# Kernel tuning notes

Measured on AMD Instinct MI355X. Metric: run time of the kernel, lower is better.

Reference implementation:

```python
import jax, jax.numpy as jnp
import numpy as np

B, S, H, A, M, V, E = 128, 64, 1000, 1000, 500, 30000, 620


def setup_inputs() -> dict:
    key = jax.random.key(0)
    ks = jax.random.split(key, 20)
    sc = 0.02
    return {
        "x": jax.random.randint(ks[0], (B, 1), 0, V),
        "hidden": jax.random.normal(ks[1], (B, H), jnp.float32),
        "outputs": jax.random.normal(ks[2], (B, S, 2 * H), jnp.float32),
        "emb": jax.random.normal(ks[3], (V, E), jnp.float32) * sc,
        "W_hp": jax.random.normal(ks[4], (A, H), jnp.float32) * sc,
        "b_hp": jnp.zeros((A,), jnp.float32),
        "W_op": jax.random.normal(ks[5], (A, 2 * H), jnp.float32) * sc,
        "b_op": jnp.zeros((A,), jnp.float32),
        "v_e": jax.random.normal(ks[6], (A,), jnp.float32) * sc,
        "W_ih": jax.random.normal(ks[7], (3 * H, 2 * H + E), jnp.float32) * sc,
        "W_hh": jax.random.normal(ks[8], (3 * H, H), jnp.float32) * sc,
        "b_ih": jnp.zeros((3 * H,), jnp.float32),
        "b_hh": jnp.zeros((3 * H,), jnp.float32),
        "W_wv": jax.random.normal(ks[9], (2 * M, 2 * H), jnp.float32) * sc,
        "b_wv": jnp.zeros((2 * M,), jnp.float32),
        "W_lh": jax.random.normal(ks[10], (2 * M, H), jnp.float32) * sc,
        "b_lh": jnp.zeros((2 * M,), jnp.float32),
        "W_le": jax.random.normal(ks[11], (2 * M, E), jnp.float32) * sc,
        "b_le": jnp.zeros((2 * M,), jnp.float32),
        "W_pred": jax.random.normal(ks[12], (V, M), jnp.float32) * sc,
        "b_pred": jnp.zeros((V,), jnp.float32),
    }


def reference(x, hidden, outputs, emb, W_hp, b_hp, W_op, b_op, v_e,
              W_ih, W_hh, b_ih, b_hh, W_wv, b_wv, W_lh, b_lh, W_le, b_le,
              W_pred, b_pred):
    # --- Bahdanau attention (broadcast instead of repeat) ---
    h_proj = hidden @ W_hp.T + b_hp                      # [B,A]
    o_proj = jnp.einsum('bsk,ak->bsa', outputs, W_op) + b_op  # [B,S,A]
    energy = jnp.tanh(h_proj[:, None, :] + o_proj) @ v_e # [B,S]
    attn = jax.nn.softmax(energy, axis=1)                # [B,S]
    ctx = jnp.einsum('bs,bsk->bk', attn, outputs)        # [B,2H] weighted_values

    # --- embedding lookup ---
    emb_x = emb[x[:, 0]]                                 # [B,E]

    # --- single-step GRU (PyTorch gate layout: r, z, n) ---
    gru_in = jnp.concatenate([emb_x, ctx], axis=1)       # [B, E+2H]
    gi = gru_in @ W_ih.T + b_ih                          # [B,3H]
    gh = hidden @ W_hh.T + b_hh                          # [B,3H]
    ir, iz, inn = gi[:, :H], gi[:, H:2*H], gi[:, 2*H:]
    hr, hz, hn = gh[:, :H], gh[:, H:2*H], gh[:, 2*H:]
    r = jax.nn.sigmoid(ir + hr)
    z = jax.nn.sigmoid(iz + hz)
    n = jnp.tanh(inn + r * hn)
    h_new = (1.0 - z) * n + z * hidden                   # [B,H]

    # --- maxout combine of three linears ---
    mo_in = (hidden @ W_lh.T + b_lh) + (emb_x @ W_le.T + b_le) + (ctx @ W_wv.T + b_wv)  # [B,2M]
    mo = mo_in.reshape(-1, M, 2).max(axis=2)             # [B,M]

    prediction = mo @ W_pred.T + b_pred                  # [B,V]
    return prediction, h_new
```

## Files before the change

### kernel.cpp

```cpp
#include <hip/hip_runtime.h>
#include <hip/hip_bf16.h>
#include <math.h>

typedef short bf16x8 __attribute__((ext_vector_type(8)));
typedef float f32x4 __attribute__((ext_vector_type(4)));
typedef unsigned short us8 __attribute__((ext_vector_type(8)));
typedef unsigned short us4 __attribute__((ext_vector_type(4)));

namespace {
constexpr int B_ = 128;
constexpr int S_ = 64;
constexpr int H_ = 1000;
constexpr int A_ = 1000;
constexpr int M_ = 500;
constexpr int V_ = 30000;
constexpr int E_ = 620;

constexpr int KP_OUT  = 2048;
constexpr int KP_HP   = 1024;
constexpr int KP_PRED = 512;
constexpr int LD_CAT  = 3712;
constexpr int NP_A    = 1024;
constexpr int NP_3H   = 3072;
constexpr int OROWS   = 8192;

constexpr int Z_HP = 4, Z_GI = 6, Z_GH = 4, Z_MO = 6, Z_OP = 2;

__device__ __forceinline__ unsigned short f2b(float f) {
  __hip_bfloat16 h = __float2bfloat16(f);
  return *reinterpret_cast<unsigned short*>(&h);
}
__device__ __forceinline__ float b2f(unsigned short u) {
  unsigned v = ((unsigned)u) << 16;
  return __uint_as_float(v);
}
__device__ __forceinline__ float sigmoidf_(float x) {
  return 1.0f / (1.0f + __expf(-x));
}
__device__ __forceinline__ void load_lds16(const void* g, void* l) {
  auto gp = reinterpret_cast<const __attribute__((address_space(1))) char*>(
      reinterpret_cast<uintptr_t>(g));
  unsigned loff = (unsigned)(uintptr_t)l;
  auto lp = reinterpret_cast<__attribute__((address_space(3))) char*>(loff);
  __builtin_amdgcn_global_load_lds(gp, lp, 16, 0, 0);
}
}

struct CJob {
  const float* src; unsigned short* dst;
  int nchunks, cpr, Kel, Rs, ld, coff, Wlim, bstart, nblk;
};

__global__ __launch_bounds__(256) void megacast(CJob j0, CJob j1, CJob j2)
{
  const int bid = blockIdx.x;
  CJob j = j0;
  if (bid >= j1.bstart) j = j1;
  if (bid >= j2.bstart) j = j2;

  const int tpj = j.nblk << 8;
  const int base = ((bid - j.bstart) << 8) + (int)threadIdx.x;

  for (int i = base; i < j.nchunks; i += tpj * 2) {
    const int i2 = i + tpj;
    const bool okB = (i2 < j.nchunks);
    const int rA = i / j.cpr;
    const int cA = (i - rA * j.cpr) << 3;
    const int rB = okB ? (i2 / j.cpr) : 0;
    const int cB = okB ? ((i2 - rB * j.cpr) << 3) : 0;
    const bool fA = (rA < j.Rs) && (cA + 8 <= j.Kel);
    const bool fB = okB && (rB < j.Rs) && (cB + 8 <= j.Kel);

    float4 a0, a1, b0, b1;
    if (fA) {
      const float* s = j.src + (size_t)rA * j.Kel + cA;
      a0 = *(const float4*)s; a1 = *(const float4*)(s + 4);
    }
    if (fB) {
      const float* s = j.src + (size_t)rB * j.Kel + cB;
      b0 = *(const float4*)s; b1 = *(const float4*)(s + 4);
    }

    if (fA) {
      us8 o;
      o[0] = f2b(a0.x); o[1] = f2b(a0.y); o[2] = f2b(a0.z); o[3] = f2b(a0.w);
      o[4] = f2b(a1.x); o[5] = f2b(a1.y); o[6] = f2b(a1.z); o[7] = f2b(a1.w);
      *(us8*)(j.dst + (size_t)rA * j.ld + j.coff + cA) = o;
    } else {
      unsigned short* drow = j.dst + (size_t)rA * j.ld + j.coff;
#pragma unroll
      for (int e = 0; e < 8; ++e) {
        const int c = cA + e;
        if (c < j.Wlim) {
          const float v = (rA < j.Rs && c < j.Kel)
                              ? j.src[(size_t)rA * j.Kel + c] : 0.f;
          drow[c] = f2b(v);
        }
      }
    }
    if (okB) {
      if (fB) {
        us8 o;
        o[0] = f2b(b0.x); o[1] = f2b(b0.y); o[2] = f2b(b0.z); o[3] = f2b(b0.w);
        o[4] = f2b(b1.x); o[5] = f2b(b1.y); o[6] = f2b(b1.z); o[7] = f2b(b1.w);
        *(us8*)(j.dst + (size_t)rB * j.ld + j.coff + cB) = o;
      } else {
        unsigned short* drow = j.dst + (size_t)rB * j.ld + j.coff;
#pragma unroll
        for (int e = 0; e < 8; ++e) {
          const int c = cB + e;
          if (c < j.Wlim) {
            const float v = (rB < j.Rs && c < j.Kel)
                                ? j.src[(size_t)rB * j.Kel + c] : 0.f;
            drow[c] = f2b(v);
          }
        }
      }
    }
  }
}

struct SJob {
  const unsigned short* A; int lda;
  const float* B; int ldb;
  int Nv, Kv;
  float* C; int ldc;
  const float* bias; int Ncol;
  int nK, Z, ntiles, bstart;
};

__global__ __launch_bounds__(256, 4) void gemm_skinny(
    SJob j0, SJob j1, SJob j2, SJob j3)
{
  __shared__ __align__(16) char Bs[2][4096];

  const int bid = blockIdx.x;
  SJob j = j0;
  if (bid >= j1.bstart) j = j1;
  if (bid >= j2.bstart) j = j2;
  if (bid >= j3.bstart) j = j3;
  const int lb = bid - j.bstart;
  const int tile = lb % j.ntiles, z = lb / j.ntiles;
  const int n0 = tile * 32;
  const int ks = (int)((long)j.nK * z / j.Z);
  const int ke = (int)((long)j.nK * (z + 1) / j.Z);

  const int t = threadIdx.x, lane = t & 63, wid = t >> 6;
  const int l15 = lane & 15, l4 = lane >> 4;
  const int mrow = (wid & 1) * 64;
  const int whalf = wid >> 1;

  const int srow = t >> 3;
  const int skq = (t & 7) * 8;
  const int grow = n0 + srow;
  const bool rowok = grow < j.Nv;
  const float* Bp = j.B + (size_t)(rowok ? grow : 0) * j.ldb;
  const unsigned swcol = (unsigned)(skq * 2) ^ (((unsigned)srow & 7u) << 4);

  const unsigned short* Arow = j.A + (size_t)(mrow + l15) * j.lda + l4 * 8;
  const int brow = whalf * 16 + l15;
  const unsigned bb = (unsigned)brow * 128;
  const unsigned bsw = (((unsigned)brow & 7u) << 4);

  float4 sf0, sf1;
  auto stage_load = [&](int kst) {
    const int gk = kst * 64 + skq;
    sf0 = make_float4(0.f, 0.f, 0.f, 0.f);
    sf1 = make_float4(0.f, 0.f, 0.f, 0.f);
    if (rowok) {
      if (gk + 8 <= j.Kv) {
        sf0 = *(const float4*)(Bp + gk);
        sf1 = *(const float4*)(Bp + gk + 4);
      } else {
        float tmp[8];
#pragma unroll
        for (int e = 0; e < 8; ++e)
          tmp[e] = (gk + e < j.Kv) ? Bp[gk + e] : 0.f;
        sf0 = make_float4(tmp[0], tmp[1], tmp[2], tmp[3]);
        sf1 = make_float4(tmp[4], tmp[5], tmp[6], tmp[7]);
      }
    }
  };
  auto stage_write = [&](int buf) {
    us8 o;
    o[0] = f2b(sf0.x); o[1] = f2b(sf0.y); o[2] = f2b(sf0.z); o[3] = f2b(sf0.w);
    o[4] = f2b(sf1.x); o[5] = f2b(sf1.y); o[6] = f2b(sf1.z); o[7] = f2b(sf1.w);
    *(us8*)((char*)Bs[buf] + srow * 128 + swcol) = o;
  };

  f32x4 acc[4] = {};
  stage_load(ks);
  stage_write(0);
  __syncthreads();

  for (int kst = ks; kst < ke; ++kst) {
    const int cur = (kst - ks) & 1;
    const bool more = (kst + 1 < ke);
    if (more) stage_load(kst + 1);
    bf16x8 Af[4][2];
#pragma unroll
    for (int kk = 0; kk < 2; ++kk)
#pragma unroll
      for (int mf = 0; mf < 4; ++mf)
        Af[mf][kk] = *(const bf16x8*)(Arow + (size_t)mf * 16 * j.lda +
                                      kst * 64 + kk * 32);
    bf16x8 Bf[2];
#pragma unroll
    for (int kk = 0; kk < 2; ++kk)
      Bf[kk] = *(const bf16x8*)((char*)Bs[cur] + bb +
                                ((unsigned)(kk * 64 + l4 * 16) ^ bsw));
#pragma unroll
    for (int kk = 0; kk < 2; ++kk)
#pragma unroll
      for (int mf = 0; mf < 4; ++mf)
        acc[mf] = __builtin_amdgcn_mfma_f32_16x16x32_bf16(Af[mf][kk], Bf[kk],
                                                          acc[mf], 0, 0, 0);
    if (more) stage_write(cur ^ 1);
    __syncthreads();
  }

  const int c = n0 + whalf * 16 + l15;
  if (j.bias) {
    if (c < j.Ncol) {
      const float bv = j.bias[c];
#pragma unroll
      for (int mf = 0; mf < 4; ++mf) {
        const int r = mrow + mf * 16 + l4 * 4;
#pragma unroll
        for (int q = 0; q < 4; ++q)
          j.C[(size_t)(r + q) * j.ldc + c] = acc[mf][q] + bv;
      }
    }
  } else {
    float* Cz = j.C + (size_t)z * 128 * j.ldc;
#pragma unroll
    for (int mf = 0; mf < 4; ++mf) {
      const int r = mrow + mf * 16 + l4 * 4;
#pragma unroll
      for (int q = 0; q < 4; ++q)
        Cz[(size_t)(r + q) * j.ldc + c] = acc[mf][q];
    }
  }
}

__global__ __launch_bounds__(256, 2) void pred_gemm(
    const unsigned short* __restrict__ mo_bf,
    const float* __restrict__ Wp,
    const float* __restrict__ bias,
    float* __restrict__ C)
{
  __shared__ __align__(16) char Bs0[32768];
  __shared__ __align__(16) char Bs1[32768];

  const int t = threadIdx.x, lane = t & 63, wid = t >> 6;
  const int l15 = lane & 15, l4 = lane >> 4;
  const int n0 = blockIdx.x * 64;
  const int mrow = wid * 32;

  bf16x8 af[2][16];
#pragma unroll
  for (int ksl = 0; ksl < 16; ++ksl)
#pragma unroll
    for (int mf = 0; mf < 2; ++mf)
      af[mf][ksl] = *(const bf16x8*)(mo_bf +
          (size_t)(mrow + mf * 16 + l15) * KP_PRED + ksl * 32 + l4 * 8);

  auto stage = [&](int st, char* buf) {
#pragma unroll
    for (int i = 0; i < 8; ++i) {
      const unsigned off = (unsigned)i * 4096 + (unsigned)t * 16;
      const unsigned row = off >> 11, colb = off & 2047u;
      const unsigned sc = colb ^ ((row & 7u) << 4);
      const int rg = n0 + st * 16 + (int)row;
      const bool ok = (rg < V_) && (sc + 16 <= 2000u);
      const char* src = ok ? ((const char*)Wp + (size_t)rg * 2000 + sc)
                           : (const char*)Wp;
      load_lds16(src, buf + off);
    }
  };

  f32x4 acc[4][2] = {};

  stage(0, Bs0);
  stage(1, Bs1);

#define PWAIT(N) do {                                              \
    asm volatile("s_waitcnt vmcnt(" #N ")" ::: "memory");          \
    __builtin_amdgcn_sched_barrier(0);                             \
    __builtin_amdgcn_s_barrier();                                  \
  } while (0)

#define PCOMPUTE(T, BUF) do {                                              \
    const char* Brow_ = (const char*)(BUF) + (unsigned)l15 * 2048;         \
    const unsigned sw_ = ((unsigned)l15 & 7u) << 4;                        \
    _Pragma("unroll")                                                      \
    for (int ksl = 0; ksl < 16; ++ksl) {                                   \
      const unsigned base_ = (unsigned)(ksl * 128 + l4 * 32);              \
      const float4 f0_ = *(const float4*)(Brow_ + (base_ ^ sw_));          \
      const float4 f1_ = *(const float4*)(Brow_ + ((base_ + 16) ^ sw_));   \
      bf16x8 bf_;                                                          \
      bf_[0] = (short)f2b(f0_.x); bf_[1] = (short)f2b(f0_.y);              \
      bf_[2] = (short)f2b(f0_.z); bf_[3] = (short)f2b(f0_.w);              \
      bf_[4] = (short)f2b(f1_.x); bf_[5] = (short)f2b(f1_.y);              \
      bf_[6] = (short)f2b(f1_.z); bf_[7] = (short)f2b(f1_.w);              \
      acc[T][0] = __builtin_amdgcn_mfma_f32_16x16x32_bf16(af[0][ksl], bf_, \
                                                          acc[T][0], 0, 0, 0); \
      acc[T][1] = __builtin_amdgcn_mfma_f32_16x16x32_bf16(af[1][ksl], bf_, \
                                                          acc[T][1], 0, 0, 0); \
    }                                                                      \
  } while (0)

  PWAIT(8);
  PCOMPUTE(0, Bs0);
  __builtin_amdgcn_s_barrier();
  stage(2, Bs0);

  PWAIT(8);
  PCOMPUTE(1, Bs1);
  __builtin_amdgcn_s_barrier();
  stage(3, Bs1);

  PWAIT(8);
  PCOMPUTE(2, Bs0);

  PWAIT(0);
  PCOMPUTE(3, Bs1);

#undef PWAIT
#undef PCOMPUTE

#pragma unroll
  for (int st = 0; st < 4; ++st) {
    const int c = n0 + st * 16 + l15;
    if (c < V_) {
      const float bv = bias[c];
#pragma unroll
      for (int mf = 0; mf < 2; ++mf) {
        const int r = mrow + mf * 16 + l4 * 4;
#pragma unroll
        for (int q = 0; q < 4; ++q)
          C[(size_t)(r + q) * V_ + c] = acc[st][mf][q] + bv;
      }
    }
  }
}

__global__ __launch_bounds__(256, 4) void gemm128_part(
    const unsigned short* __restrict__ Abf, int ldA,
    const unsigned short* __restrict__ Bbf, int ldB,
    unsigned short* __restrict__ Cout, int ldc, int nK)
{
  __shared__ __align__(16) char As[16384];
  __shared__ __align__(16) char Bs[16384];

  const int t = threadIdx.x;
  const int lane = t & 63, wid = t >> 6;
  const int wm = wid >> 1, wn = wid & 1;
  const int l15 = lane & 15, l4 = lane >> 4;
  const int m0 = blockIdx.x * 128;
  const int n0 = blockIdx.y * 128;
  const int z = blockIdx.z, Z = gridDim.z;
  const int ks = (int)((long)nK * z / Z), ke = (int)((long)nK * (z + 1) / Z);

  f32x4 acc[4][4] = {};

  for (int kst = ks; kst < ke; ++kst) {
    const int k0 = kst * 64;
#pragma unroll
    for (int c = 0; c < 4; ++c) {
      const unsigned ou = c * 4096 + wid * 1024;
      const unsigned oo = ou + lane * 16;
      const unsigned row = oo >> 7, cb = oo & 127u;
      const unsigned scb = cb ^ ((row & 7u) << 4);
      load_lds16((const char*)Abf + ((size_t)(m0 + row) * ldA + k0) * 2 + scb,
                 As + ou);
    }
#pragma unroll
    for (int c = 0; c < 4; ++c) {
      const unsigned ou = c * 4096 + wid * 1024;
      const unsigned oo = ou + lane * 16;
      const unsigned row = oo >> 7, cb = oo & 127u;
      const unsigned scb = cb ^ ((row & 7u) << 4);
      load_lds16((const char*)Bbf + ((size_t)(n0 + row) * ldB + k0) * 2 + scb,
                 Bs + ou);
    }
    __syncthreads();

#pragma unroll
    for (int kk = 0; kk < 2; ++kk) {
      bf16x8 af[4], bfr[4];
#pragma unroll
      for (int i = 0; i < 4; ++i) {
        const unsigned ra = wm * 64 + i * 16 + l15;
        const unsigned ca = (unsigned)(kk * 64 + l4 * 16) ^ ((ra & 7u) << 4);
        af[i] = *(const bf16x8*)(As + ra * 128 + ca);
        const unsigned rb = wn * 64 + i * 16 + l15;
        const unsigned cb2 = (unsigned)(kk * 64 + l4 * 16) ^ ((rb & 7u) << 4);
        bfr[i] = *(const bf16x8*)(Bs + rb * 128 + cb2);
      }
#pragma unroll
      for (int i = 0; i < 4; ++i)
#pragma unroll
        for (int jj = 0; jj < 4; ++jj)
          acc[i][jj] = __builtin_amdgcn_mfma_f32_16x16x32_bf16(af[i], bfr[jj],
                                                               acc[i][jj], 0, 0, 0);
    }
    __syncthreads();
  }

  unsigned short* Cz = Cout + (size_t)z * OROWS * ldc;
#pragma unroll
  for (int i = 0; i < 4; ++i) {
    const int r = m0 + wm * 64 + i * 16 + l4 * 4;
#pragma unroll
    for (int jj = 0; jj < 4; ++jj) {
      const int c = n0 + wn * 64 + jj * 16 + l15;
#pragma unroll
      for (int q = 0; q < 4; ++q)
        Cz[(size_t)(r + q) * ldc + c] = f2b(acc[i][jj][q]);
    }
  }
}

__global__ __launch_bounds__(256) void hp_combine(
    const float* __restrict__ hp, const float* __restrict__ b_op,
    const float* __restrict__ b_hp, float* __restrict__ hpc)
{
  const int idx = blockIdx.x * 256 + threadIdx.x;
  if (idx >= B_ * NP_A) return;
  const int c = idx & (NP_A - 1);
  float s = (c < A_) ? (b_op[c] + b_hp[c]) : 0.f;
#pragma unroll
  for (int zz = 0; zz < Z_HP; ++zz) s += hp[(size_t)zz * B_ * NP_A + idx];
  hpc[idx] = s;
}

__global__ __launch_bounds__(256) void energy_reduce(
    const unsigned short* __restrict__ opart, const float* __restrict__ hpc,
    const float* __restrict__ ve, float* __restrict__ energy)
{
  const int r = blockIdx.x;
  const int b = r >> 6;
  const int t = threadIdx.x;
  float s = 0.f;
  if (t < 250) {
    const int c0 = t * 4;
    const us4 v0 = *(const us4*)(opart + (size_t)r * NP_A + c0);
    const us4 v1 = *(const us4*)(opart + (size_t)OROWS * NP_A + (size_t)r * NP_A + c0);
    const float4 h = *(const float4*)(hpc + (size_t)b * NP_A + c0);
    const float4 vv = *(const float4*)(ve + c0);
    s = tanhf(b2f(v0[0]) + b2f(v1[0]) + h.x) * vv.x
      + tanhf(b2f(v0[1]) + b2f(v1[1]) + h.y) * vv.y
      + tanhf(b2f(v0[2]) + b2f(v1[2]) + h.z) * vv.z
      + tanhf(b2f(v0[3]) + b2f(v1[3]) + h.w) * vv.w;
  }
#pragma unroll
  for (int w = 1; w < 64; w <<= 1) s += __shfl_xor(s, w);
  __shared__ float red[4];
  if ((t & 63) == 0) red[t >> 6] = s;
  __syncthreads();
  if (t == 0) energy[r] = red[0] + red[1] + red[2] + red[3];
}

__global__ __launch_bounds__(256) void softmax_ctx_cat(
    const float* __restrict__ energy, const unsigned short* __restrict__ outb,
    const float* __restrict__ hidden, const float* __restrict__ emb,
    const int* __restrict__ x, unsigned short* __restrict__ cat3)
{
  const int b = blockIdx.x, yq = blockIdx.y;
  const int t = threadIdx.x;
  __shared__ float attn[S_];
  __shared__ float sinv_s;

  if (t < 64) {
    const float e = energy[b * S_ + t];
    float m = e;
#pragma unroll
    for (int w = 1; w < 64; w <<= 1) m = fmaxf(m, __shfl_xor(m, w));
    const float p = __expf(e - m);
    float s = p;
#pragma unroll
    for (int w = 1; w < 64; w <<= 1) s += __shfl_xor(s, w);
    attn[t] = p;
    if (t == 0) sinv_s = 1.f / s;
  }
  __syncthreads();
  const float inv = sinv_s;
  unsigned short* catb = cat3 + (size_t)b * LD_CAT;

  {
    const int c0 = (250 * yq) / 4, c1 = (250 * (yq + 1)) / 4;
    const unsigned short* ob = outb + (size_t)b * S_ * KP_OUT;
    for (int kk = c0 + t; kk < c1; kk += 256) {
      float a[8] = {0.f, 0.f, 0.f, 0.f, 0.f, 0.f, 0.f, 0.f};
      for (int s = 0; s < S_; ++s) {
        const float w = attn[s];
        const us8 v = *(const us8*)(ob + (size_t)s * KP_OUT + kk * 8);
#pragma unroll
        for (int jj = 0; jj < 8; ++jj) a[jj] = fmaf(w, b2f(v[jj]), a[jj]);
      }
      us4 lo, hi;
#pragma unroll
      for (int jj = 0; jj < 4; ++jj) {
        lo[jj] = f2b(a[jj] * inv); hi[jj] = f2b(a[jj + 4] * inv);
      }
      *(us4*)(catb + 1620 + kk * 8) = lo;
      *(us4*)(catb + 1620 + kk * 8 + 4) = hi;
    }
  }
  {
    const int c0 = (250 * yq) / 4, c1 = (250 * (yq + 1)) / 4;
    for (int kk = c0 + t; kk < c1; kk += 256) {
      const float4 f = *(const float4*)(hidden + (size_t)b * H_ + kk * 4);
      us4 v; v[0] = f2b(f.x); v[1] = f2b(f.y); v[2] = f2b(f.z); v[3] = f2b(f.w);
      *(us4*)(catb + kk * 4) = v;
    }
  }
  {
    const int xi = x[b];
    const int c0 = (155 * yq) / 4, c1 = (155 * (yq + 1)) / 4;
    for (int kk = c0 + t; kk < c1; kk += 256) {
      const float4 f = *(const float4*)(emb + (size_t)xi * E_ + kk * 4);
      us4 v; v[0] = f2b(f.x); v[1] = f2b(f.y); v[2] = f2b(f.z); v[3] = f2b(f.w);
      *(us4*)(catb + 1000 + kk * 4) = v;
    }
  }
  if (yq == 3) {
    for (int kk = t; kk < 23; kk += 256) {
      us4 v; v[0] = 0; v[1] = 0; v[2] = 0; v[3] = 0;
      *(us4*)(catb + 3620 + kk * 4) = v;
    }
  }
}

__global__ __launch_bounds__(256) void gru_combine(
    const float* __restrict__ gi, const float* __restrict__ gh,
    const float* __restrict__ b_ih, const float* __restrict__ b_hh,
    const float* __restrict__ hidden, float* __restrict__ hout)
{
  const int idx = blockIdx.x * 256 + threadIdx.x;
  if (idx >= B_ * H_) return;
  const int b = idx / H_, h = idx - b * H_;
  float ir = b_ih[h], iz = b_ih[H_ + h], in = b_ih[2 * H_ + h];
  float hr = b_hh[h], hz = b_hh[H_ + h], hn = b_hh[2 * H_ + h];
#pragma unroll
  for (int zz = 0; zz < Z_GI; ++zz) {
    const float* g = gi + (size_t)zz * B_ * NP_3H + (size_t)b * NP_3H;
    ir += g[h]; iz += g[H_ + h]; in += g[2 * H_ + h];
  }
#pragma unroll
  for (int zz = 0; zz < Z_GH; ++zz) {
    const float* g = gh + (size_t)zz * B_ * NP_3H + (size_t)b * NP_3H;
    hr += g[h]; hz += g[H_ + h]; hn += g[2 * H_ + h];
  }
  const float r = sigmoidf_(ir + hr);
  const float zg = sigmoidf_(iz + hz);
  const float n = tanhf(in + r * hn);
  hout[idx] = (1.f - zg) * n + zg * hidden[idx];
}

__global__ __launch_bounds__(256) void maxpair_cast(
    const float* __restrict__ mo_in,
    const float* __restrict__ b_lh, const float* __restrict__ b_le,
    const float* __restrict__ b_wv, unsigned short* __restrict__ mo_bf)
{
  const int idx = blockIdx.x * 256 + threadIdx.x;
  if (idx >= B_ * KP_PRED) return;
  const int r = idx >> 9, c = idx & 511;
  unsigned short o = 0;
  if (c < M_) {
    const int j0 = 2 * c, j1 = 2 * c + 1;
    float v0 = b_lh[j0] + b_le[j0] + b_wv[j0];
    float v1 = b_lh[j1] + b_le[j1] + b_wv[j1];
#pragma unroll
    for (int zz = 0; zz < Z_MO; ++zz) {
      const float* g = mo_in + (size_t)zz * B_ * NP_A + (size_t)r * NP_A;
      v0 += g[j0]; v1 += g[j1];
    }
    o = f2b(fmaxf(v0, v1));
  }
  mo_bf[idx] = o;
}

extern "C" void kernel_launch(void* const* d_in, const int* in_sizes, int n_in,
                              void* d_out, int out_size, void* d_ws, size_t ws_size,
                              hipStream_t stream)
{
  const int*   x       = (const int*)  d_in[0];
  const float* hidden  = (const float*)d_in[1];
  const float* outputs = (const float*)d_in[2];
  const float* emb     = (const float*)d_in[3];
  const float* W_hp    = (const float*)d_in[4];
  const float* b_hp    = (const float*)d_in[5];
  const float* W_op    = (const float*)d_in[6];
  const float* b_op    = (const float*)d_in[7];
  const float* v_e     = (const float*)d_in[8];
  const float* W_ih    = (const float*)d_in[9];
  const float* W_hh    = (const float*)d_in[10];
  const float* b_ih    = (const float*)d_in[11];
  const float* b_hh    = (const float*)d_in[12];
  const float* W_wv    = (const float*)d_in[13];
  const float* b_wv    = (const float*)d_in[14];
  const float* W_lh    = (const float*)d_in[15];
  const float* b_lh    = (const float*)d_in[16];
  const float* W_le    = (const float*)d_in[17];
  const float* b_le    = (const float*)d_in[18];
  const float* W_pred  = (const float*)d_in[19];
  const float* b_pred  = (const float*)d_in[20];

  char* w = (char*)d_ws;
  auto alloc = [&](size_t bytes) {
    char* p = w; w += (bytes + 255) & ~(size_t)255; return p;
  };
  unsigned short* outputs_bf = (unsigned short*)alloc((size_t)OROWS * KP_OUT * 2);
  unsigned short* W_op_bf    = (unsigned short*)alloc((size_t)NP_A * KP_OUT * 2);
  unsigned short* hidden_bf  = (unsigned short*)alloc((size_t)B_ * KP_HP * 2);
  unsigned short* cat3_bf    = (unsigned short*)alloc((size_t)B_ * LD_CAT * 2);
  unsigned short* mo_bf      = (unsigned short*)alloc((size_t)B_ * KP_PRED * 2);
  float* hp     = (float*)alloc((size_t)Z_HP * B_ * NP_A * 4);
  float* hpc    = (float*)alloc((size_t)B_ * NP_A * 4);
  float* energy = (float*)alloc((size_t)B_ * S_ * 4);
  float* gh     = (float*)alloc((size_t)Z_GH * B_ * NP_3H * 4);
  char* un = w;
  unsigned short* opart = (unsigned short*)un;
  float* gi     = (float*)un;
  float* mo_in  = gi + (size_t)Z_GI * B_ * NP_3H;

  float* pred = (float*)d_out;
  float* hout = pred + (size_t)B_ * V_;

  const dim3 blk(256);
  const int FAR = 0x7fffffff;
  const SJob dummy = { nullptr, 0, nullptr, 0, 0, 0, nullptr, 0,
                       nullptr, 0, 1, 1, 1, FAR };

  {
    CJob jo  = { outputs, outputs_bf, OROWS * 256, 256, 2000, OROWS,
                 KP_OUT, 0, KP_OUT, 0,    2560 };
    CJob jwo = { W_op,    W_op_bf,    NP_A * 256,  256, 2000, A_,
                 KP_OUT, 0, KP_OUT, 2560, 320 };
    CJob jh  = { hidden,  hidden_bf,  B_ * 128,    128, 1000, B_,
                 KP_HP,  0, KP_HP,  2880, 32 };
    megacast<<<dim3(2912), blk, 0, stream>>>(jo, jwo, jh);
  }

  {
    SJob jhp = { hidden_bf, KP_HP, W_hp, H_, A_, H_, hp, NP_A,
                 nullptr, 0, 16, Z_HP, 32, 0 };
    SJob jgh = { hidden_bf, KP_HP, W_hh, H_, 3 * H_, H_, gh, NP_3H,
                 nullptr, 0, 16, Z_GH, 94, 128 };
    gemm_skinny<<<dim3(504), blk, 0, stream>>>(jhp, jgh, dummy, dummy);
  }
  hp_combine<<<dim3(B_ * NP_A / 256), blk, 0, stream>>>(hp, b_op, b_hp, hpc);

  gemm128_part<<<dim3(64, 8, Z_OP), blk, 0, stream>>>(
      outputs_bf, KP_OUT, W_op_bf, KP_OUT, opart, NP_A, KP_OUT / 64);

  energy_reduce<<<dim3(OROWS), blk, 0, stream>>>(opart, hpc, v_e, energy);

  softmax_ctx_cat<<<dim3(B_, 4), blk, 0, stream>>>(
      energy, outputs_bf, hidden, emb, x, cat3_bf);

  {
    SJob jgi = { cat3_bf + 1000, LD_CAT, W_ih, 2620, 3 * H_, 2620, gi, NP_3H,
                 nullptr, 0, 41, Z_GI, 94, 0 };
    SJob jlh = { cat3_bf, LD_CAT, W_lh, H_, A_, H_,
                 mo_in, NP_A, nullptr, 0, 16, 2, 32, 564 };
    SJob jle = { cat3_bf + 1000, LD_CAT, W_le, E_, A_, E_,
                 mo_in + (size_t)2 * B_ * NP_A, NP_A, nullptr, 0, 10, 1, 32, 628 };
    SJob jwv = { cat3_bf + 1620, LD_CAT, W_wv, 2 * H_, A_, 2 * H_,
                 mo_in + (size_t)3 * B_ * NP_A, NP_A, nullptr, 0, 32, 3, 32, 660 };
    gemm_skinny<<<dim3(756), blk, 0, stream>>>(jgi, jlh, jle, jwv);
  }

  gru_combine<<<dim3((B_ * H_ + 255) / 256), blk, 0, stream>>>(
      gi, gh, b_ih, b_hh, hidden, hout);

  maxpair_cast<<<dim3((B_ * KP_PRED + 255) / 256), blk, 0, stream>>>(
      mo_in, b_lh, b_le, b_wv, mo_bf);

  pred_gemm<<<dim3(469), blk, 0, stream>>>(mo_bf, W_pred, b_pred, pred);
}
```

Before: 161.3 us.

## Double-buffer LDS tiles in gemm128_part to overlap global loads with MFMA

Turns the split-K bf16 GEMM's single LDS buffer into two and prefetches the tile for step k+2 while step k is computed. Explicit vmcnt waits and raw s_barrier replace __syncthreads, so the load of the next tile stays in flight. LDS use per block doubles to 64KB, which lowers occupancy (launch bounds drop from 4 to 2 blocks per CU). The code always issues stage(ks+1) even when the range holds a single k-step, which could read past the intended slice.

```diff
diff --git a/kernel.cpp b/kernel.cpp
--- a/kernel.cpp
+++ b/kernel.cpp
@@ -345,13 +345,13 @@
   }
 }
 
-__global__ __launch_bounds__(256, 4) void gemm128_part(
+__global__ __launch_bounds__(256, 2) void gemm128_part(
     const unsigned short* __restrict__ Abf, int ldA,
     const unsigned short* __restrict__ Bbf, int ldB,
     unsigned short* __restrict__ Cout, int ldc, int nK)
 {
-  __shared__ __align__(16) char As[16384];
-  __shared__ __align__(16) char Bs[16384];
+  __shared__ __align__(16) char As[2][16384];
+  __shared__ __align__(16) char Bs[2][16384];
 
   const int t = threadIdx.x;
   const int lane = t & 63, wid = t >> 6;
@@ -362,9 +362,7 @@
   const int z = blockIdx.z, Z = gridDim.z;
   const int ks = (int)((long)nK * z / Z), ke = (int)((long)nK * (z + 1) / Z);
 
-  f32x4 acc[4][4] = {};
-
-  for (int kst = ks; kst < ke; ++kst) {
+  auto stage = [&](int kst, int p) {
     const int k0 = kst * 64;
 #pragma unroll
     for (int c = 0; c < 4; ++c) {
@@ -373,18 +371,26 @@
       const unsigned row = oo >> 7, cb = oo & 127u;
       const unsigned scb = cb ^ ((row & 7u) << 4);
       load_lds16((const char*)Abf + ((size_t)(m0 + row) * ldA + k0) * 2 + scb,
-                 As + ou);
-    }
-#pragma unroll
-    for (int c = 0; c < 4; ++c) {
-      const unsigned ou = c * 4096 + wid * 1024;
-      const unsigned oo = ou + lane * 16;
-      const unsigned row = oo >> 7, cb = oo & 127u;
-      const unsigned scb = cb ^ ((row & 7u) << 4);
+                 As[p] + ou);
       load_lds16((const char*)Bbf + ((size_t)(n0 + row) * ldB + k0) * 2 + scb,
-                 Bs + ou);
-    }
-    __syncthreads();
+                 Bs[p] + ou);
+    }
+  };
+
+  f32x4 acc[4][4] = {};
+
+  stage(ks, 0);
+  stage(ks + 1, 1);
+
+  for (int kst = ks; kst < ke; ++kst) {
+    const int cur = (kst - ks) & 1;
+    if (kst + 1 < ke) {
+      asm volatile("s_waitcnt vmcnt(8)" ::: "memory");
+    } else {
+      asm volatile("s_waitcnt vmcnt(0)" ::: "memory");
+    }
+    __builtin_amdgcn_sched_barrier(0);
+    __builtin_amdgcn_s_barrier();
 
 #pragma unroll
     for (int kk = 0; kk < 2; ++kk) {
@@ -393,10 +399,10 @@
       for (int i = 0; i < 4; ++i) {
         const unsigned ra = wm * 64 + i * 16 + l15;
         const unsigned ca = (unsigned)(kk * 64 + l4 * 16) ^ ((ra & 7u) << 4);
-        af[i] = *(const bf16x8*)(As + ra * 128 + ca);
+        af[i] = *(const bf16x8*)(As[cur] + ra * 128 + ca);
         const unsigned rb = wn * 64 + i * 16 + l15;
         const unsigned cb2 = (unsigned)(kk * 64 + l4 * 16) ^ ((rb & 7u) << 4);
-        bfr[i] = *(const bf16x8*)(Bs + rb * 128 + cb2);
+        bfr[i] = *(const bf16x8*)(Bs[cur] + rb * 128 + cb2);
       }
 #pragma unroll
       for (int i = 0; i < 4; ++i)
@@ -405,7 +411,8 @@
           acc[i][jj] = __builtin_amdgcn_mfma_f32_16x16x32_bf16(af[i], bfr[jj],
                                                                acc[i][jj], 0, 0, 0);
     }
-    __syncthreads();
+    __builtin_amdgcn_s_barrier();
+    if (kst + 2 < ke) stage(kst + 2, cur);
   }
 
   unsigned short* Cz = Cout + (size_t)z * OROWS * ldc;
```

Result: no change. 162.0 us (+0.4%).
